# Kernel tuning notes

Hardware: AMD Instinct MI355X
Metric: run time of the kernel (lower is better)

Reference implementation:

```python
import jax, jax.numpy as jnp
import numpy as np

D_EMB = 1024
N_HEAD = 16
D_K = D_EMB // N_HEAD


def setup_inputs() -> dict:
    key = jax.random.key(0)
    ks = jax.random.split(key, 11)
    B, S = 2, 2048
    s = 1.0 / np.sqrt(D_EMB)
    inp = {
        'Q': jax.random.normal(ks[0], (B, S, D_EMB), jnp.float32),
        'K': jax.random.normal(ks[1], (B, S, D_EMB), jnp.float32),
        'V': jax.random.normal(ks[2], (B, S, D_EMB), jnp.float32),
        'W_Q': jax.random.normal(ks[3], (D_EMB, D_EMB), jnp.float32) * s,
        'b_Q': jax.random.normal(ks[4], (D_EMB,), jnp.float32) * s,
        'W_K': jax.random.normal(ks[5], (D_EMB, D_EMB), jnp.float32) * s,
        'b_K': jax.random.normal(ks[6], (D_EMB,), jnp.float32) * s,
        'W_V': jax.random.normal(ks[7], (D_EMB, D_EMB), jnp.float32) * s,
        'b_V': jax.random.normal(ks[8], (D_EMB,), jnp.float32) * s,
        'W_O': jax.random.normal(ks[9], (D_EMB, D_EMB), jnp.float32) * s,
        'b_O': jax.random.normal(ks[10], (D_EMB,), jnp.float32) * s,
    }
    return inp


def _heads(x):
    # [B, S, D] -> [B, H, S, d_k]
    B, S, _ = x.shape
    return x.reshape(B, S, N_HEAD, D_K).transpose(0, 2, 1, 3)


def reference(Q, K, V, W_Q, b_Q, W_K, b_K, W_V, b_V, W_O, b_O):
    q = _heads(Q @ W_Q.T + b_Q)
    k = _heads(K @ W_K.T + b_K)
    v = _heads(V @ W_V.T + b_V)
    scale = 1.0 / jnp.sqrt(jnp.asarray(D_K, q.dtype))
    scores = jnp.einsum('bhqd,bhkd->bhqk', q, k) * scale  # [B,H,S,S]
    probs = jax.nn.softmax(scores, axis=-1)
    attn = jnp.einsum('bhqk,bhkd->bhqd', probs, v)
    B, H, S, d = attn.shape
    attn = attn.transpose(0, 2, 1, 3).reshape(B, S, H * d)
    return attn @ W_O.T + b_O
```

## Files before the change

kernel.cpp:

```cpp
#include <hip/hip_runtime.h>
#include <cstdint>
#include <cstddef>

#define S_LEN 2048
#define NH    16
#define DKH   64
#define DEMB  1024
#define MTOT  4096

typedef float f32x4 __attribute__((ext_vector_type(4)));
typedef __bf16 bf16x8 __attribute__((ext_vector_type(8)));
typedef unsigned short u16;
typedef unsigned int u32;
typedef u16 u16x8 __attribute__((ext_vector_type(8)));
typedef u16 u16x4 __attribute__((ext_vector_type(4)));

static __device__ __forceinline__ u16 f2bf(float f) {
  u32 u = __builtin_bit_cast(u32, f);
  u += 0x7fffu + ((u >> 16) & 1u);
  return (u16)(u >> 16);
}
static __device__ __forceinline__ bf16x8 ldfrag(const u16* p) {
  return __builtin_bit_cast(bf16x8, *(const u16x8*)p);
}
static __device__ __forceinline__ f32x4 mfma16(bf16x8 a, bf16x8 b, f32x4 c) {
  return __builtin_amdgcn_mfma_f32_16x16x32_bf16(a, b, c, 0, 0, 0);
}
static __device__ __forceinline__ void gl2lds16(const void* g, void* l) {
  __builtin_amdgcn_global_load_lds((__attribute__((address_space(1))) void*)g,
                                   (__attribute__((address_space(3))) void*)l,
                                   16, 0, 0);
}

#define SCL_Q (0.125f * 1.44269504088896340736f)

__global__ __launch_bounds__(256) void cvt_bf16(const float* __restrict__ s,
                                                u16* __restrict__ d, int n) {
  int i = (blockIdx.x * 256 + threadIdx.x) * 4;
  if (i >= n) return;
  f32x4 f = *(const f32x4*)(s + i);
  u16x4 o;
  o[0] = f2bf(f[0]); o[1] = f2bf(f[1]); o[2] = f2bf(f[2]); o[3] = f2bf(f[3]);
  *(u16x4*)(d + i) = o;
}

__global__ __launch_bounds__(256) void qkv_gemm(
    const u16* __restrict__ qin, const u16* __restrict__ kin,
    const u16* __restrict__ vin, const u16* __restrict__ W,
    const float* __restrict__ bq, const float* __restrict__ bk,
    const float* __restrict__ bv,
    u16* __restrict__ qh, u16* __restrict__ kh, u16* __restrict__ vt) {
  __shared__ __align__(16) u16 sA[128 * 32];
  __shared__ __align__(16) u16 sB[128 * 32];
  const int t = threadIdx.x;
  const int l = t & 63, w = t >> 6;
  const int ll = l & 15, lg = l >> 4;
  const int nb = blockIdx.x;
  const int mb = blockIdx.y;
  const int which = nb >> 3;
  const u16* A = (which == 0) ? qin : ((which == 1) ? kin : vin);
  const int wr = (w >> 1) * 64, wc = (w & 1) * 64;

  f32x4 acc[4][4] = {};

  for (int kt = 0; kt < 32; ++kt) {
    const int k0 = kt * 32;
    __syncthreads();
#pragma unroll
    for (int i = 0; i < 2; ++i) {
      const int c = i * 256 + t;
      const int row = c >> 2;
      const int gc = (c & 3) ^ ((row >> 1) & 3);
      gl2lds16(A + (size_t)(mb * 128 + row) * DEMB + k0 + gc * 8, &sA[c * 8]);
      gl2lds16(W + (size_t)(nb * 128 + row) * DEMB + k0 + gc * 8, &sB[c * 8]);
    }
    __syncthreads();

    bf16x8 af[4], bfr[4];
#pragma unroll
    for (int i2 = 0; i2 < 4; ++i2) {
      const int row = wr + i2 * 16 + ll;
      af[i2] = ldfrag(&sA[row * 32 + (lg ^ ((row >> 1) & 3)) * 8]);
    }
#pragma unroll
    for (int j2 = 0; j2 < 4; ++j2) {
      const int row = wc + j2 * 16 + ll;
      bfr[j2] = ldfrag(&sB[row * 32 + (lg ^ ((row >> 1) & 3)) * 8]);
    }
#pragma unroll
    for (int i2 = 0; i2 < 4; ++i2)
#pragma unroll
      for (int j2 = 0; j2 < 4; ++j2)
        acc[i2][j2] = mfma16(af[i2], bfr[j2], acc[i2][j2]);
  }

  const float* bias = (which == 0) ? bq : ((which == 1) ? bk : bv);
  const int b = (mb * 128) >> 11;

  if (which == 2) {
#pragma unroll
    for (int j2 = 0; j2 < 4; ++j2) {
      const int nl = (nb * 128 + wc + j2 * 16 + ll) & 1023;
      const int h = nl >> 6, dk = nl & 63;
      const float bb = bias[nl];
      u16* base = vt + ((size_t)((b * NH + h) * DKH + dk)) * S_LEN;
#pragma unroll
      for (int i2 = 0; i2 < 4; ++i2) {
        const int s = (mb * 128 + wr + i2 * 16 + lg * 4) & 2047;
        u16x4 pk;
#pragma unroll
        for (int r = 0; r < 4; ++r) pk[r] = f2bf(acc[i2][j2][r] + bb);
        *(u16x4*)&base[s] = pk;
      }
    }
  } else {
    u16* outp = (which == 0) ? qh : kh;
    const float scl = (which == 0) ? SCL_Q : 1.0f;
#pragma unroll
    for (int j2 = 0; j2 < 4; ++j2) {
      const int nl = (nb * 128 + wc + j2 * 16 + ll) & 1023;
      const int h = nl >> 6, dk = nl & 63;
      const float bb = bias[nl];
#pragma unroll
      for (int i2 = 0; i2 < 4; ++i2) {
#pragma unroll
        for (int r = 0; r < 4; ++r) {
          const int s = (mb * 128 + wr + i2 * 16 + lg * 4 + r) & 2047;
          const float val = (acc[i2][j2][r] + bb) * scl;
          outp[((size_t)((b * NH + h) * S_LEN + s)) * DKH + dk] = f2bf(val);
        }
      }
    }
  }
}

__global__ __launch_bounds__(256) void attn_kernel(
    const u16* __restrict__ qh, const u16* __restrict__ kh,
    const u16* __restrict__ vt, u16* __restrict__ ctx) {
  __shared__ __align__(16) u16 sK[128 * 64];
  __shared__ __align__(16) u16 sV[64 * 128];
  __shared__ __align__(16) u16 sP[4][2][16 * 128];
  const int t = threadIdx.x;
  const int l = t & 63, w = t >> 6;
  const int ll = l & 15, lg = l >> 4;
  const int q_blk = blockIdx.x * 128;
  const int bh = blockIdx.y;

  bf16x8 aq[2][2];
#pragma unroll
  for (int qt = 0; qt < 2; ++qt) {
    const u16* qbase = qh + ((size_t)bh * S_LEN + q_blk + w * 32 + qt * 16 + ll) * DKH;
    aq[qt][0] = ldfrag(qbase + lg * 8);
    aq[qt][1] = ldfrag(qbase + 32 + lg * 8);
  }

  f32x4 oT[2][4] = {};
  float l_part[2] = {0.f, 0.f};

  u16* sP0 = &sP[w][0][0];
  u16* sP1 = &sP[w][1][0];

  for (int kt = 0; kt < 16; ++kt) {
    __syncthreads();
#pragma unroll
    for (int i = 0; i < 4; ++i) {
      const int c = i * 256 + t;
      {
        const int row = c >> 3, gc = (c & 7) ^ (row & 7);
        gl2lds16(kh + ((size_t)bh * S_LEN + kt * 128 + row) * DKH + gc * 8,
                 &sK[c * 8]);
      }
      {
        const int row = c >> 4, gc = (c & 15) ^ (row & 15);
        gl2lds16(vt + ((size_t)bh * DKH + row) * S_LEN + kt * 128 + gc * 8,
                 &sV[c * 8]);
      }
    }
    __syncthreads();

#pragma unroll
    for (int kb = 0; kb < 8; ++kb) {
      const int krow = kb * 16 + ll;
      const bf16x8 ak0 = ldfrag(&sK[krow * 64 + (lg ^ (ll & 7)) * 8]);
      const bf16x8 ak1 = ldfrag(&sK[krow * 64 + ((4 + lg) ^ (ll & 7)) * 8]);
      f32x4 s0 = {}, s1 = {};
      s0 = mfma16(ak0, aq[0][0], s0);
      s0 = mfma16(ak1, aq[0][1], s0);
      s1 = mfma16(ak0, aq[1][0], s1);
      s1 = mfma16(ak1, aq[1][1], s1);
      const int poff = ll * 128 + ((kb ^ (ll & 7)) * 4 + lg) * 4;
      u16x4 pk;
      float ps = 0.f;
#pragma unroll
      for (int r = 0; r < 4; ++r) {
        const float p = __builtin_amdgcn_exp2f(s0[r]);
        ps += p; pk[r] = f2bf(p);
      }
      l_part[0] += ps;
      *(u16x4*)&sP0[poff] = pk;
      ps = 0.f;
#pragma unroll
      for (int r = 0; r < 4; ++r) {
        const float p = __builtin_amdgcn_exp2f(s1[r]);
        ps += p; pk[r] = f2bf(p);
      }
      l_part[1] += ps;
      *(u16x4*)&sP1[poff] = pk;
    }

    bf16x8 bp0[4], bp1[4];
#pragma unroll
    for (int f = 0; f < 4; ++f) {
      const int kb = f * 2 + (lg >> 1);
      const int off = ll * 128 + ((kb ^ (ll & 7)) * 4 + 2 * (lg & 1)) * 4;
      bp0[f] = ldfrag(&sP0[off]);
      bp1[f] = ldfrag(&sP1[off]);
    }
#pragma unroll
    for (int nt = 0; nt < 4; ++nt) {
      const int vrow = nt * 16 + ll;
#pragma unroll
      for (int f = 0; f < 4; ++f) {
        const bf16x8 av = ldfrag(&sV[vrow * 128 + ((f * 4 + lg) ^ ll) * 8]);
        oT[0][nt] = mfma16(av, bp0[f], oT[0][nt]);
        oT[1][nt] = mfma16(av, bp1[f], oT[1][nt]);
      }
    }
  }

  const int b = bh >> 4, h = bh & 15;
#pragma unroll
  for (int qt = 0; qt < 2; ++qt) {
    float lv = l_part[qt];
    lv += __shfl_xor(lv, 16, 64);
    lv += __shfl_xor(lv, 32, 64);
    const float inv = 1.0f / lv;
    const int srow = q_blk + w * 32 + qt * 16 + ll;
#pragma unroll
    for (int nt = 0; nt < 4; ++nt) {
      u16x4 o;
#pragma unroll
      for (int r = 0; r < 4; ++r) o[r] = f2bf(oT[qt][nt][r] * inv);
      *(u16x4*)&ctx[((size_t)((b * S_LEN + srow) * NH + h)) * DKH + nt * 16 + lg * 4] = o;
    }
  }
}

__global__ __launch_bounds__(256) void out_gemm(
    const u16* __restrict__ Am, const u16* __restrict__ W,
    const float* __restrict__ bo, float* __restrict__ out) {
  __shared__ __align__(16) u16 sA[64 * 64];
  __shared__ __align__(16) u16 sB[64 * 64];
  const int t = threadIdx.x;
  const int l = t & 63, w = t >> 6;
  const int ll = l & 15, lg = l >> 4;
  const int nb = blockIdx.x;
  const int mb = blockIdx.y;
  const int wr = (w >> 1) * 32, wc = (w & 1) * 32;

  f32x4 acc[2][2] = {};
  for (int kt = 0; kt < 16; ++kt) {
    const int k0 = kt * 64;
    __syncthreads();
#pragma unroll
    for (int i = 0; i < 2; ++i) {
      const int c = i * 256 + t;
      const int row = c >> 3;
      const int gc = (c & 7) ^ (row & 7);
      gl2lds16(Am + (size_t)(mb * 64 + row) * DEMB + k0 + gc * 8, &sA[c * 8]);
      gl2lds16(W + (size_t)(nb * 64 + row) * DEMB + k0 + gc * 8, &sB[c * 8]);
    }
    __syncthreads();
#pragma unroll
    for (int sub = 0; sub < 2; ++sub) {
      bf16x8 af[2], bfr[2];
#pragma unroll
      for (int i2 = 0; i2 < 2; ++i2) {
        const int row = wr + i2 * 16 + ll;
        af[i2] = ldfrag(&sA[row * 64 + ((sub * 4 + lg) ^ (row & 7)) * 8]);
      }
#pragma unroll
      for (int j2 = 0; j2 < 2; ++j2) {
        const int row = wc + j2 * 16 + ll;
        bfr[j2] = ldfrag(&sB[row * 64 + ((sub * 4 + lg) ^ (row & 7)) * 8]);
      }
#pragma unroll
      for (int i2 = 0; i2 < 2; ++i2)
#pragma unroll
        for (int j2 = 0; j2 < 2; ++j2)
          acc[i2][j2] = mfma16(af[i2], bfr[j2], acc[i2][j2]);
    }
  }

#pragma unroll
  for (int j2 = 0; j2 < 2; ++j2) {
    const int ncol = nb * 64 + wc + j2 * 16 + ll;
    const float bb = bo[ncol];
#pragma unroll
    for (int i2 = 0; i2 < 2; ++i2) {
#pragma unroll
      for (int r = 0; r < 4; ++r) {
        const int mrow = mb * 64 + wr + i2 * 16 + lg * 4 + r;
        out[(size_t)mrow * DEMB + ncol] = acc[i2][j2][r] + bb;
      }
    }
  }
}

extern "C" void kernel_launch(void* const* d_in, const int* in_sizes, int n_in,
                              void* d_out, int out_size, void* d_ws,
                              size_t ws_size, hipStream_t stream) {
  (void)in_sizes; (void)n_in; (void)out_size; (void)ws_size;
  const float* Q  = (const float*)d_in[0];
  const float* K  = (const float*)d_in[1];
  const float* V  = (const float*)d_in[2];
  const float* WQ = (const float*)d_in[3];
  const float* bQ = (const float*)d_in[4];
  const float* WK = (const float*)d_in[5];
  const float* bK = (const float*)d_in[6];
  const float* WV = (const float*)d_in[7];
  const float* bV = (const float*)d_in[8];
  const float* WO = (const float*)d_in[9];
  const float* bO = (const float*)d_in[10];
  float* out = (float*)d_out;

  u16* ws   = (u16*)d_ws;
  u16* Wqkv = ws;
  u16* Wo   = Wqkv + 3072 * 1024;
  u16* qin  = Wo + 1024 * 1024;
  u16* kin  = qin + (size_t)MTOT * DEMB;
  u16* vin  = kin + (size_t)MTOT * DEMB;
  u16* qh   = vin + (size_t)MTOT * DEMB;
  u16* kh   = qh + 32 * 2048 * 64;
  u16* vt   = kh + 32 * 2048 * 64;
  u16* ctx  = vt + 32 * 2048 * 64;

  const int WN = DEMB * DEMB;
  const int AN = MTOT * DEMB;
  cvt_bf16<<<WN / 1024, 256, 0, stream>>>(WQ, Wqkv, WN);
  cvt_bf16<<<WN / 1024, 256, 0, stream>>>(WK, Wqkv + WN, WN);
  cvt_bf16<<<WN / 1024, 256, 0, stream>>>(WV, Wqkv + 2 * WN, WN);
  cvt_bf16<<<WN / 1024, 256, 0, stream>>>(WO, Wo, WN);
  cvt_bf16<<<AN / 1024, 256, 0, stream>>>(Q, qin, AN);
  cvt_bf16<<<AN / 1024, 256, 0, stream>>>(K, kin, AN);
  cvt_bf16<<<AN / 1024, 256, 0, stream>>>(V, vin, AN);

  qkv_gemm<<<dim3(24, 32), 256, 0, stream>>>(qin, kin, vin, Wqkv, bQ, bK, bV,
                                             qh, kh, vt);
  attn_kernel<<<dim3(16, 32), 256, 0, stream>>>(qh, kh, vt, ctx);
  out_gemm<<<dim3(16, 64), 256, 0, stream>>>(ctx, Wo, bO, out);
}
```

Before: 257.1 us.

## Split attention P tile into halves with padded LDS and cheaper bf16 packing

The 128-key tile's score/exp/PV work is split into two 64-key halves, so each warp's P buffer shrinks from 16x128 to a padded 16x68 layout. This cuts LDS usage, which may let more blocks fit per CU, and overlaps the exp work of one half with the PV MFMAs of the other. The round-to-nearest-even bf16 conversion is replaced by a round-half-up add plus v_perm packing, which is fewer instructions but rounds ties slightly differently. P fragments are read back as two 8-byte loads per fragment instead of one 16-byte load, adding some LDS instructions.

```diff
diff --git a/kernel.cpp b/kernel.cpp
--- a/kernel.cpp
+++ b/kernel.cpp
@@ -14,6 +14,7 @@
 typedef unsigned int u32;
 typedef u16 u16x8 __attribute__((ext_vector_type(8)));
 typedef u16 u16x4 __attribute__((ext_vector_type(4)));
+typedef u32 u32x2 __attribute__((ext_vector_type(2)));
 
 static __device__ __forceinline__ u16 f2bf(float f) {
   u32 u = __builtin_bit_cast(u32, f);
@@ -30,6 +31,11 @@
   __builtin_amdgcn_global_load_lds((__attribute__((address_space(1))) void*)g,
                                    (__attribute__((address_space(3))) void*)l,
                                    16, 0, 0);
+}
+static __device__ __forceinline__ u32 pkbf(float hi, float lo) {
+  u32 a = __builtin_bit_cast(u32, hi) + 0x8000u;
+  u32 b = __builtin_bit_cast(u32, lo) + 0x8000u;
+  return __builtin_amdgcn_perm(a, b, 0x07060302u);
 }
 
 #define SCL_Q (0.125f * 1.44269504088896340736f)
@@ -139,7 +145,7 @@
     const u16* __restrict__ vt, u16* __restrict__ ctx) {
   __shared__ __align__(16) u16 sK[128 * 64];
   __shared__ __align__(16) u16 sV[64 * 128];
-  __shared__ __align__(16) u16 sP[4][2][16 * 128];
+  __shared__ __align__(16) u16 sP[4][2][16 * 68];
   const int t = threadIdx.x;
   const int l = t & 63, w = t >> 6;
   const int ll = l & 15, lg = l >> 4;
@@ -179,51 +185,62 @@
     __syncthreads();
 
 #pragma unroll
-    for (int kb = 0; kb < 8; ++kb) {
-      const int krow = kb * 16 + ll;
-      const bf16x8 ak0 = ldfrag(&sK[krow * 64 + (lg ^ (ll & 7)) * 8]);
-      const bf16x8 ak1 = ldfrag(&sK[krow * 64 + ((4 + lg) ^ (ll & 7)) * 8]);
-      f32x4 s0 = {}, s1 = {};
-      s0 = mfma16(ak0, aq[0][0], s0);
-      s0 = mfma16(ak1, aq[0][1], s0);
-      s1 = mfma16(ak0, aq[1][0], s1);
-      s1 = mfma16(ak1, aq[1][1], s1);
-      const int poff = ll * 128 + ((kb ^ (ll & 7)) * 4 + lg) * 4;
-      u16x4 pk;
-      float ps = 0.f;
-#pragma unroll
-      for (int r = 0; r < 4; ++r) {
-        const float p = __builtin_amdgcn_exp2f(s0[r]);
-        ps += p; pk[r] = f2bf(p);
-      }
-      l_part[0] += ps;
-      *(u16x4*)&sP0[poff] = pk;
-      ps = 0.f;
-#pragma unroll
-      for (int r = 0; r < 4; ++r) {
-        const float p = __builtin_amdgcn_exp2f(s1[r]);
-        ps += p; pk[r] = f2bf(p);
-      }
-      l_part[1] += ps;
-      *(u16x4*)&sP1[poff] = pk;
-    }
-
-    bf16x8 bp0[4], bp1[4];
-#pragma unroll
-    for (int f = 0; f < 4; ++f) {
-      const int kb = f * 2 + (lg >> 1);
-      const int off = ll * 128 + ((kb ^ (ll & 7)) * 4 + 2 * (lg & 1)) * 4;
-      bp0[f] = ldfrag(&sP0[off]);
-      bp1[f] = ldfrag(&sP1[off]);
-    }
-#pragma unroll
-    for (int nt = 0; nt < 4; ++nt) {
-      const int vrow = nt * 16 + ll;
-#pragma unroll
-      for (int f = 0; f < 4; ++f) {
-        const bf16x8 av = ldfrag(&sV[vrow * 128 + ((f * 4 + lg) ^ ll) * 8]);
-        oT[0][nt] = mfma16(av, bp0[f], oT[0][nt]);
-        oT[1][nt] = mfma16(av, bp1[f], oT[1][nt]);
+    for (int h = 0; h < 2; ++h) {
+#pragma unroll
+      for (int kbl = 0; kbl < 4; ++kbl) {
+        const int kb = h * 4 + kbl;
+        const int krow = kb * 16 + ll;
+        const bf16x8 ak0 = ldfrag(&sK[krow * 64 + (lg ^ (ll & 7)) * 8]);
+        const bf16x8 ak1 = ldfrag(&sK[krow * 64 + ((4 + lg) ^ (ll & 7)) * 8]);
+        f32x4 s0 = {}, s1 = {};
+        s0 = mfma16(ak0, aq[0][0], s0);
+        s0 = mfma16(ak1, aq[0][1], s0);
+        s1 = mfma16(ak0, aq[1][0], s1);
+        s1 = mfma16(ak1, aq[1][1], s1);
+        const int poff = ll * 68 + kbl * 16 + lg * 4;
+        {
+          const float p0 = __builtin_amdgcn_exp2f(s0[0]);
+          const float p1 = __builtin_amdgcn_exp2f(s0[1]);
+          const float p2 = __builtin_amdgcn_exp2f(s0[2]);
+          const float p3 = __builtin_amdgcn_exp2f(s0[3]);
+          l_part[0] += (p0 + p1) + (p2 + p3);
+          u32x2 pk; pk[0] = pkbf(p1, p0); pk[1] = pkbf(p3, p2);
+          *(u32x2*)&sP0[poff] = pk;
+        }
+        {
+          const float p0 = __builtin_amdgcn_exp2f(s1[0]);
+          const float p1 = __builtin_amdgcn_exp2f(s1[1]);
+          const float p2 = __builtin_amdgcn_exp2f(s1[2]);
+          const float p3 = __builtin_amdgcn_exp2f(s1[3]);
+          l_part[1] += (p0 + p1) + (p2 + p3);
+          u32x2 pk; pk[0] = pkbf(p1, p0); pk[1] = pkbf(p3, p2);
+          *(u32x2*)&sP1[poff] = pk;
+        }
+      }
+
+      bf16x8 bp[2][2];
+#pragma unroll
+      for (int fl = 0; fl < 2; ++fl) {
+        const int off = ll * 68 + fl * 32 + lg * 8;
+        const u16x4 lo0 = *(const u16x4*)&sP0[off];
+        const u16x4 hi0 = *(const u16x4*)&sP0[off + 4];
+        bp[0][fl] = __builtin_bit_cast(bf16x8,
+            __builtin_shufflevector(lo0, hi0, 0, 1, 2, 3, 4, 5, 6, 7));
+        const u16x4 lo1 = *(const u16x4*)&sP1[off];
+        const u16x4 hi1 = *(const u16x4*)&sP1[off + 4];
+        bp[1][fl] = __builtin_bit_cast(bf16x8,
+            __builtin_shufflevector(lo1, hi1, 0, 1, 2, 3, 4, 5, 6, 7));
+      }
+#pragma unroll
+      for (int nt = 0; nt < 4; ++nt) {
+        const int vrow = nt * 16 + ll;
+#pragma unroll
+        for (int fl = 0; fl < 2; ++fl) {
+          const int fg = h * 2 + fl;
+          const bf16x8 av = ldfrag(&sV[vrow * 128 + ((fg * 4 + lg) ^ ll) * 8]);
+          oT[0][nt] = mfma16(av, bp[0][fl], oT[0][nt]);
+          oT[1][nt] = mfma16(av, bp[1][fl], oT[1][nt]);
+        }
       }
     }
   }
```

Result: faster. 250.1 us (-2.7%).
